# Kernel optimization log

Hardware: AMD Instinct MI355X
Metric: run time of the kernel (lower is better)

Reference implementation:

```python
import jax, jax.numpy as jnp
import numpy as np

TOP_K = 2  # moe_top_k


def setup_inputs() -> dict:
    key = jax.random.key(0)
    k0, k1, k2, k3 = jax.random.split(key, 4)
    SL, BS, H, F, E = 2048, 4, 1024, 1024, 8
    x = jax.random.normal(k0, (SL, BS, H), dtype=jnp.float32)
    w_router = jax.random.normal(k1, (H, E), dtype=jnp.float32) * 0.02
    w1 = jax.random.normal(k2, (E, H, F), dtype=jnp.float32) * 0.02  # per-expert map weights
    w2 = jax.random.normal(k3, (E, F, H), dtype=jnp.float32) * 0.02  # per-expert reduce weights
    return {"x": x, "w_router": w_router, "w1": w1, "w2": w2}


def reference(x, w_router, w1, w2):
    # dMoA forward: router -> dropless dispatch -> per-expert map GEMM ->
    # per-expert reduce GEMM -> expert-weighted combine. Dropless = no capacity
    # dropping, so a dense all-experts compute + per-token selection is exactly
    # equivalent in math to the sort/gather/grouped-GEMM/scatter pipeline.
    sl, bs, h = x.shape
    E = w1.shape[0]
    xt = x.reshape(-1, h)  # [T, H], T = sl*bs
    T = xt.shape[0]

    # LearnedRouter: softmax over expert logits, then top-k weights/indices
    scores = jax.nn.softmax(xt @ w_router, axis=-1)       # [T, E]
    expert_weights, top_experts = jax.lax.top_k(scores, TOP_K)  # [T, K]

    # load-balancing loss (router.loss): E * sum_e f_e * p_e
    onehot = jax.nn.one_hot(top_experts, E, dtype=xt.dtype)  # [T, K, E]
    tokens_frac = onehot.sum(axis=(0, 1)) / (T * TOP_K)      # f_e
    probs_mean = scores.mean(axis=0)                         # p_e
    loss = E * jnp.sum(tokens_frac * probs_mean)

    # map: per-expert linear H->F, select the top-k experts' outputs per token
    y_all = jnp.einsum('th,ehf->tef', xt, w1)                 # [T, E, F]
    h_tk = jnp.take_along_axis(y_all, top_experts[:, :, None], axis=1)  # [T, K, F]

    # reduce: weighted scatter-combine, then per-expert linear F->H
    hw = jnp.einsum('tke,tk,tkf->tef', onehot, expert_weights, h_tk)  # [T, E, F]
    out = jnp.einsum('tef,efh->th', hw, w2)                   # [T, H]
    return out.reshape(sl, bs, h), loss
```

## Files before the change

### kernel.cpp

```cpp
#include <hip/hip_runtime.h>
#include <hip/hip_bf16.h>
#include <stdint.h>


#define HD 1024
#define FD 1024
#define EN 8

typedef __attribute__((ext_vector_type(8))) short bf16x8;
typedef __attribute__((ext_vector_type(4))) float f32x4;

__device__ __forceinline__ void gload16(const void* g, void* l) {
    __builtin_amdgcn_global_load_lds(
        (const __attribute__((address_space(1))) unsigned int*)g,
        (__attribute__((address_space(3))) unsigned int*)l, 16, 0, 0);
}

__device__ __forceinline__ ushort f2bf(float v) {
    __hip_bfloat16 h = __float2bfloat16(v);
    return *(ushort*)&h;
}
__device__ __forceinline__ float bf2f(ushort u) {
    unsigned int w = ((unsigned int)u) << 16;
    float f; __builtin_memcpy(&f, &w, 4); return f;
}

__global__ __launch_bounds__(256) void router_kernel(
    const float* __restrict__ x, const float* __restrict__ wrt,
    ushort* __restrict__ xb,
    int* __restrict__ top_e, float* __restrict__ top_w,
    int* __restrict__ counts, float* __restrict__ probsum)
{
    __shared__ int   cnt_s[EN];
    __shared__ float ps_s[EN];
    int tid = threadIdx.x;
    if (tid < EN) { cnt_s[tid] = 0; ps_s[tid] = 0.f; }
    __syncthreads();

    int wid = tid >> 6, lane = tid & 63;
    int t = blockIdx.x * 4 + wid;
    const float4* xr4 = (const float4*)(x + (size_t)t * HD);
    ushort4* xbo = (ushort4*)(xb + (size_t)t * HD);
    float acc[EN];
#pragma unroll
    for (int e = 0; e < EN; e++) acc[e] = 0.f;
#pragma unroll
    for (int it = 0; it < 4; it++) {
        float4 xv = xr4[it * 64 + lane];
        ushort4 o; o.x = f2bf(xv.x); o.y = f2bf(xv.y); o.z = f2bf(xv.z); o.w = f2bf(xv.w);
        xbo[it * 64 + lane] = o;
        int h0 = it * 256 + lane * 4;
        float xs[4] = {xv.x, xv.y, xv.z, xv.w};
#pragma unroll
        for (int j = 0; j < 4; j++) {
            const float4* wp = (const float4*)(wrt + (size_t)(h0 + j) * EN);
            float4 wa = wp[0], wb = wp[1];
            acc[0] += xs[j] * wa.x; acc[1] += xs[j] * wa.y;
            acc[2] += xs[j] * wa.z; acc[3] += xs[j] * wa.w;
            acc[4] += xs[j] * wb.x; acc[5] += xs[j] * wb.y;
            acc[6] += xs[j] * wb.z; acc[7] += xs[j] * wb.w;
        }
    }
#pragma unroll
    for (int off = 32; off >= 1; off >>= 1) {
#pragma unroll
        for (int e = 0; e < EN; e++) acc[e] += __shfl_xor(acc[e], off, 64);
    }
    if (lane == 0) {
        float m = acc[0];
#pragma unroll
        for (int e = 1; e < EN; e++) m = fmaxf(m, acc[e]);
        float p[EN], s = 0.f;
#pragma unroll
        for (int e = 0; e < EN; e++) { p[e] = expf(acc[e] - m); s += p[e]; }
        float inv = 1.f / s;
#pragma unroll
        for (int e = 0; e < EN; e++) p[e] *= inv;
        int e0 = 0;
#pragma unroll
        for (int e = 1; e < EN; e++) if (p[e] > p[e0]) e0 = e;
        int e1 = (e0 == 0) ? 1 : 0;
#pragma unroll
        for (int e = 0; e < EN; e++) {
            if (e == e0) continue;
            if (p[e] > p[e1]) e1 = e;
        }
        top_e[t * 2] = e0;  top_e[t * 2 + 1] = e1;
        top_w[t * 2] = p[e0]; top_w[t * 2 + 1] = p[e1];
        atomicAdd(&cnt_s[e0], 1); atomicAdd(&cnt_s[e1], 1);
#pragma unroll
        for (int e = 0; e < EN; e++) atomicAdd(&ps_s[e], p[e]);
    }
    __syncthreads();
    if (tid < EN) {
        atomicAdd(&counts[tid], cnt_s[tid]);
        atomicAdd(&probsum[tid], ps_s[tid]);
    }
}

__global__ void prep_kernel(const int* __restrict__ counts,
                            const float* __restrict__ probsum,
                            int* __restrict__ offs, float* __restrict__ loss_out)
{
    int off = 0; float loss = 0.f;
    for (int e = 0; e < EN; e++) {
        offs[e] = off;
        off += counts[e];
        loss += ((float)counts[e] / 16384.f) * (probsum[e] / 8192.f);
    }
    offs[EN] = off;
    *loss_out = 8.f * loss;
}

__global__ __launch_bounds__(256) void dispatch_kernel(
    const int* __restrict__ top_e, const float* __restrict__ top_w,
    const int* __restrict__ offs, int* __restrict__ cursor,
    int* __restrict__ tok_list, float* __restrict__ w_list)
{
    int t = blockIdx.x * 256 + threadIdx.x;
    int lane = threadIdx.x & 63;
#pragma unroll
    for (int k = 0; k < 2; k++) {
        int e = top_e[t * 2 + k];
        int idx = 0;
#pragma unroll
        for (int ex = 0; ex < EN; ex++) {
            unsigned long long m = __ballot(e == ex);
            if (e == ex) {
                int cnt = __popcll(m);
                int leader = __ffsll(m) - 1;
                int pos = 0;
                if (lane == leader) pos = atomicAdd(&cursor[ex * 16], cnt);
                pos = __shfl(pos, leader, 64);
                int rank = __popcll(m & ((1ull << lane) - 1ull));
                idx = offs[ex] + pos + rank;
            }
        }
        tok_list[idx] = t * 2 + k;
        w_list[idx] = top_w[t * 2 + k];
    }
}

__global__ __launch_bounds__(256) void transpose_conv_kernel(
    const float* __restrict__ w1, const float* __restrict__ w2,
    ushort* __restrict__ w1b, ushort* __restrict__ w2b)
{
    __shared__ float tile[32][33];
    int bid = blockIdx.x;
    const float* in; ushort* outp;
    if (bid >= 8192) { in = w2; outp = w2b; bid -= 8192; }
    else             { in = w1; outp = w1b; }
    int e  = bid >> 10;
    int t2 = bid & 1023;
    int tb = t2 >> 5;
    int ta = t2 & 31;
    const float* pin = in + ((size_t)e << 20);
    ushort* pout = outp + ((size_t)e << 20);
    int tx = threadIdx.x & 31, ty = threadIdx.x >> 5;
#pragma unroll
    for (int j = 0; j < 4; j++)
        tile[ty + j * 8][tx] = pin[(size_t)(ta * 32 + ty + j * 8) * 1024 + tb * 32 + tx];
    __syncthreads();
#pragma unroll
    for (int j = 0; j < 4; j++)
        pout[(size_t)(tb * 32 + ty + j * 8) * 1024 + ta * 32 + tx] =
            f2bf(tile[tx][ty + j * 8]);
}


__global__ __launch_bounds__(512, 2) void map_gemm(
    const ushort* __restrict__ xb, const ushort* __restrict__ w1b,
    ushort* __restrict__ hbuf,
    const int* __restrict__ tok_list, const float* __restrict__ w_list,
    const int* __restrict__ offs)
{
    __shared__ __align__(16) short lA[2][256][64];
    __shared__ __align__(16) short lB[2][256][64];
    __shared__ int   tok_s[256];
    __shared__ float wt_s[256];

    int g = blockIdx.x;
    int e = g & 7, q = g >> 3, nb = q & 3, rb = q >> 2;
    int base = offs[e], cnt = offs[e + 1] - base;
    int row0 = rb << 8;
    if (row0 >= cnt) return;
    int rem = cnt - row0;
    int tid = threadIdx.x;
    if (tid < 256) {
        int r = row0 + tid; if (r > cnt - 1) r = cnt - 1;
        tok_s[tid] = tok_list[base + r];
        wt_s[tid]  = w_list[base + r];
    }
    __syncthreads();

    int lane = tid & 63, w = tid >> 6;
    int wm = w >> 2, wn = w & 3;
    int w32 = w * 32;
    int lr = lane >> 3;
    int kseg = ((lane & 7) ^ lr) << 3;

    const ushort* pA[4]; const ushort* pB[4];
    const ushort* wbase = w1b + ((size_t)e << 20);
#pragma unroll
    for (int i = 0; i < 4; i++) {
        int rowT = w32 + i * 8 + lr;
        pA[i] = xb + (size_t)(tok_s[rowT] >> 1) * HD + kseg;
        pB[i] = wbase + (size_t)(nb * 256 + rowT) * HD + kseg;
    }

    f32x4 acc[8][4];
#pragma unroll
    for (int m = 0; m < 8; m++)
#pragma unroll
        for (int n = 0; n < 4; n++) acc[m][n] = (f32x4){0.f, 0.f, 0.f, 0.f};

#pragma unroll
    for (int i = 0; i < 4; i++) {
        gload16(pA[i], &lA[0][w32 + i * 8][0]);
        gload16(pB[i], &lB[0][w32 + i * 8][0]);
        pA[i] += 64; pB[i] += 64;
    }
    __syncthreads();

    int lo = lane & 15, hi = lane >> 4, rx = lane & 7;
    for (int t = 0; t < 16; ++t) {
        int cur = t & 1;
        if (t < 15) {
            int nxt = cur ^ 1;
#pragma unroll
            for (int i = 0; i < 4; i++) {
                gload16(pA[i], &lA[nxt][w32 + i * 8][0]);
                gload16(pB[i], &lB[nxt][w32 + i * 8][0]);
                pA[i] += 64; pB[i] += 64;
            }
        }
#pragma unroll
        for (int ks = 0; ks < 2; ks++) {
            bf16x8 af[8], bg[4];
#pragma unroll
            for (int m = 0; m < 8; m++)
                af[m] = *(const bf16x8*)&lA[cur][wm * 128 + m * 16 + lo][((ks * 4 + hi) ^ rx) << 3];
#pragma unroll
            for (int n = 0; n < 4; n++)
                bg[n] = *(const bf16x8*)&lB[cur][wn * 64 + n * 16 + lo][((ks * 4 + hi) ^ rx) << 3];
#pragma unroll
            for (int m = 0; m < 8; m++)
#pragma unroll
                for (int n = 0; n < 4; n++)
                    acc[m][n] = __builtin_amdgcn_mfma_f32_16x16x32_bf16(af[m], bg[n], acc[m][n], 0, 0, 0);
        }
        __syncthreads();
    }

    short* ep = (w < 4 ? (short*)lA : (short*)lB) + (w & 3) * 8192;
#pragma unroll
    for (int m = 0; m < 8; m++)
#pragma unroll
        for (int r = 0; r < 4; r++) {
            int row_l = m * 16 + hi * 4 + r;
            int rswz = (row_l & 7) << 4;
            float wgt = wt_s[wm * 128 + row_l];
#pragma unroll
            for (int n = 0; n < 4; n++) {
                int colb = (n * 16 + lo) * 2;
                ep[(row_l * 128 + (colb ^ rswz)) >> 1] = f2bf(acc[m][n][r] * wgt);
            }
        }
    __syncthreads();
    size_t outbase = (size_t)(base + row0);
    int colg0 = (nb << 8) + wn * 64;
#pragma unroll
    for (int j = 0; j < 16; j++) {
        int row_l = j * 8 + (lane >> 3);
        int r_blk = wm * 128 + row_l;
        int sb = ((lane & 7) * 16) ^ ((row_l & 7) << 4);
        bf16x8 v = *(const bf16x8*)&ep[(row_l * 128 + sb) >> 1];
        if (r_blk < rem)
            *(bf16x8*)&hbuf[(outbase + r_blk) * FD + colg0 + (lane & 7) * 8] = v;
    }
}

__global__ __launch_bounds__(512, 2) void reduce_gemm(
    const ushort* __restrict__ hbuf, const ushort* __restrict__ w2b,
    ushort* __restrict__ obuf,
    const int* __restrict__ tok_list, const int* __restrict__ offs)
{
    __shared__ __align__(16) short lA[2][256][64];
    __shared__ __align__(16) short lB[2][256][64];
    __shared__ int tok_s[256];

    int g = blockIdx.x;
    int e = g & 7, q = g >> 3, nb = q & 3, rb = q >> 2;
    int base = offs[e], cnt = offs[e + 1] - base;
    int row0 = rb << 8;
    if (row0 >= cnt) return;
    int rem = cnt - row0;
    int tid = threadIdx.x;
    if (tid < 256) {
        int r = row0 + tid; if (r > cnt - 1) r = cnt - 1;
        tok_s[tid] = tok_list[base + r];
    }
    __syncthreads();

    int lane = tid & 63, w = tid >> 6;
    int wm = w >> 2, wn = w & 3;
    int w32 = w * 32;
    int lr = lane >> 3;
    int kseg = ((lane & 7) ^ lr) << 3;

    const ushort* pA[4]; const ushort* pB[4];
    const ushort* wbase = w2b + ((size_t)e << 20);
#pragma unroll
    for (int i = 0; i < 4; i++) {
        int rowT = w32 + i * 8 + lr;
        int ar = row0 + rowT; if (ar > cnt - 1) ar = cnt - 1;
        pA[i] = hbuf + (size_t)(base + ar) * FD + kseg;
        pB[i] = wbase + (size_t)(nb * 256 + rowT) * FD + kseg;
    }

    f32x4 acc[8][4];
#pragma unroll
    for (int m = 0; m < 8; m++)
#pragma unroll
        for (int n = 0; n < 4; n++) acc[m][n] = (f32x4){0.f, 0.f, 0.f, 0.f};

#pragma unroll
    for (int i = 0; i < 4; i++) {
        gload16(pA[i], &lA[0][w32 + i * 8][0]);
        gload16(pB[i], &lB[0][w32 + i * 8][0]);
        pA[i] += 64; pB[i] += 64;
    }
    __syncthreads();

    int lo = lane & 15, hi = lane >> 4, rx = lane & 7;
    for (int t = 0; t < 16; ++t) {
        int cur = t & 1;
        if (t < 15) {
            int nxt = cur ^ 1;
#pragma unroll
            for (int i = 0; i < 4; i++) {
                gload16(pA[i], &lA[nxt][w32 + i * 8][0]);
                gload16(pB[i], &lB[nxt][w32 + i * 8][0]);
                pA[i] += 64; pB[i] += 64;
            }
        }
#pragma unroll
        for (int ks = 0; ks < 2; ks++) {
            bf16x8 af[8], bg[4];
#pragma unroll
            for (int m = 0; m < 8; m++)
                af[m] = *(const bf16x8*)&lA[cur][wm * 128 + m * 16 + lo][((ks * 4 + hi) ^ rx) << 3];
#pragma unroll
            for (int n = 0; n < 4; n++)
                bg[n] = *(const bf16x8*)&lB[cur][wn * 64 + n * 16 + lo][((ks * 4 + hi) ^ rx) << 3];
#pragma unroll
            for (int m = 0; m < 8; m++)
#pragma unroll
                for (int n = 0; n < 4; n++)
                    acc[m][n] = __builtin_amdgcn_mfma_f32_16x16x32_bf16(af[m], bg[n], acc[m][n], 0, 0, 0);
        }
        __syncthreads();
    }

    short* ep = (w < 4 ? (short*)lA : (short*)lB) + (w & 3) * 8192;
#pragma unroll
    for (int m = 0; m < 8; m++)
#pragma unroll
        for (int r = 0; r < 4; r++) {
            int row_l = m * 16 + hi * 4 + r;
            int rswz = (row_l & 7) << 4;
#pragma unroll
            for (int n = 0; n < 4; n++) {
                int colb = (n * 16 + lo) * 2;
                ep[(row_l * 128 + (colb ^ rswz)) >> 1] = f2bf(acc[m][n][r]);
            }
        }
    __syncthreads();
    int colg0 = (nb << 8) + wn * 64;
#pragma unroll
    for (int j = 0; j < 16; j++) {
        int row_l = j * 8 + (lane >> 3);
        int r_blk = wm * 128 + row_l;
        int sb = ((lane & 7) * 16) ^ ((row_l & 7) << 4);
        bf16x8 v = *(const bf16x8*)&ep[(row_l * 128 + sb) >> 1];
        if (r_blk < rem)
            *(bf16x8*)&obuf[(size_t)tok_s[r_blk] * HD + colg0 + (lane & 7) * 8] = v;
    }
}

__global__ __launch_bounds__(256) void combine_kernel(
    const ushort* __restrict__ obuf, float* __restrict__ out)
{
    int g = blockIdx.x * 256 + threadIdx.x;
    int t = g >> 7, c8 = (g & 127) << 3;
    const ushort* p = obuf + (size_t)t * 2048 + c8;
    bf16x8 a = *(const bf16x8*)p;
    bf16x8 b = *(const bf16x8*)(p + 1024);
    float o[8];
#pragma unroll
    for (int i = 0; i < 8; i++)
        o[i] = bf2f((ushort)a[i]) + bf2f((ushort)b[i]);
    float* q = out + (size_t)t * HD + c8;
    *(float4*)q       = (float4){o[0], o[1], o[2], o[3]};
    *(float4*)(q + 4) = (float4){o[4], o[5], o[6], o[7]};
}

extern "C" void kernel_launch(void* const* d_in, const int* in_sizes, int n_in,
                              void* d_out, int out_size, void* d_ws, size_t ws_size,
                              hipStream_t stream)
{
    const float* x   = (const float*)d_in[0];
    const float* wrt = (const float*)d_in[1];
    const float* w1  = (const float*)d_in[2];
    const float* w2  = (const float*)d_in[3];
    float* out = (float*)d_out;

    uint8_t* ws = (uint8_t*)d_ws;
    ushort* xb   = (ushort*)(ws);
    ushort* w1b  = (ushort*)(ws + (16u << 20));
    ushort* obuf = (ushort*)(ws);
    ushort* w2b  = (ushort*)(ws + (32u << 20));
    ushort* hbuf = (ushort*)(ws + (48u << 20));
    uint8_t* p80 = ws + (80u << 20);
    int*   tok_list = (int*)(p80);
    float* w_list   = (float*)(p80 + (64u << 10));
    int*   top_e    = (int*)(p80 + (128u << 10));
    float* top_w    = (float*)(p80 + (192u << 10));
    uint8_t* ctr    = p80 + (256u << 10);
    int*   counts   = (int*)(ctr);
    float* probsum  = (float*)(ctr + 64);
    int*   offs     = (int*)(ctr + 128);
    int*   cursor   = (int*)(ctr + 256);
    float* loss_out = out + 8388608;

    hipMemsetAsync(ctr, 0, 1024, stream);

    router_kernel<<<2048, 256, 0, stream>>>(x, wrt, xb, top_e, top_w, counts, probsum);
    prep_kernel<<<1, 1, 0, stream>>>(counts, probsum, offs, loss_out);
    dispatch_kernel<<<32, 256, 0, stream>>>(top_e, top_w, offs, cursor, tok_list, w_list);
    transpose_conv_kernel<<<16384, 256, 0, stream>>>(w1, w2, w1b, w2b);
    map_gemm<<<1024, 512, 0, stream>>>(xb, w1b, hbuf, tok_list, w_list, offs);
    reduce_gemm<<<1024, 512, 0, stream>>>(hbuf, w2b, obuf, tok_list, offs);
    combine_kernel<<<4096, 256, 0, stream>>>(obuf, out);
}
```

Measured before the change: 225.4 us.

## Deepen GEMM pipeline to 4-stage K=32 ring with explicit waitcnt scheduling

Both the map and reduce grouped GEMMs change from a 2-stage double buffer with K=64 tiles to a 4-deep ring of K=32 stages. Three stages are kept in flight and each step waits on vmcnt with an explicit barrier. The inner step uses inline ds_read_b128, sched_barriers, and s_setprio around the MFMA bursts so that LDS reads interleave with matrix work and global loads stay hidden. A new XOR swizzle matches the 32-element row layout. The hand scheduling removes compiler freedom and depends on the vmcnt counts being exact.

```diff
diff --git a/kernel.cpp b/kernel.cpp
--- a/kernel.cpp
+++ b/kernel.cpp
@@ -14,6 +14,14 @@
     __builtin_amdgcn_global_load_lds(
         (const __attribute__((address_space(1))) unsigned int*)g,
         (__attribute__((address_space(3))) unsigned int*)l, 16, 0, 0);
+}
+
+__device__ __forceinline__ bf16x8 ds_read128(const short* p) {
+    bf16x8 r;
+    asm volatile("ds_read_b128 %0, %1"
+                 : "=v"(r)
+                 : "v"((const __attribute__((address_space(3))) short*)p));
+    return r;
 }
 
 __device__ __forceinline__ ushort f2bf(float v) {
@@ -168,14 +176,51 @@
 }
 
 
+#define RDA_(r_, m_) ds_read128((const short*)&L[r_][0][wm * 128 + (m_) * 16 + lo][pslot])
+#define RDB_(r_, n_) ds_read128((const short*)&L[r_][1][wn * 64  + (n_) * 16 + lo][pslot])
+
+#define STAGE(h_) do {                                                        \
+    int r_ = (h_) & 3; int ko_ = (h_) << 5;                                   \
+    gload16(pA0 + ko_, &L[r_][0][w16][0]);                                    \
+    gload16(pA1 + ko_, &L[r_][0][128 + w16][0]);                              \
+    gload16(pB0 + ko_, &L[r_][1][w16][0]);                                    \
+    gload16(pB1 + ko_, &L[r_][1][128 + w16][0]);                              \
+} while (0)
+
+#define KHALF(r_, VMSTR) do {                                                 \
+    asm volatile("s_waitcnt vmcnt(" VMSTR ")" ::: "memory");                  \
+    __builtin_amdgcn_s_barrier();                                             \
+    __builtin_amdgcn_sched_barrier(0);                                        \
+    _Pragma("unroll") for (int m = 0; m < 4; m++) a[m] = RDA_(r_, m);         \
+    _Pragma("unroll") for (int n = 0; n < 4; n++) b[n] = RDB_(r_, n);         \
+    asm volatile("s_waitcnt lgkmcnt(0)");                                     \
+    __builtin_amdgcn_sched_barrier(0);                                        \
+    __builtin_amdgcn_s_setprio(1);                                            \
+    _Pragma("unroll") for (int m = 0; m < 4; m++)                             \
+    _Pragma("unroll") for (int n = 0; n < 4; n++)                             \
+        acc[m][n] = __builtin_amdgcn_mfma_f32_16x16x32_bf16(a[m], b[n], acc[m][n], 0, 0, 0); \
+    __builtin_amdgcn_s_setprio(0);                                            \
+    __builtin_amdgcn_sched_barrier(0);                                        \
+    _Pragma("unroll") for (int m = 0; m < 4; m++) a[m] = RDA_(r_, m + 4);     \
+    asm volatile("s_waitcnt lgkmcnt(0)");                                     \
+    __builtin_amdgcn_sched_barrier(0);                                        \
+    __builtin_amdgcn_s_setprio(1);                                            \
+    _Pragma("unroll") for (int m = 0; m < 4; m++)                             \
+    _Pragma("unroll") for (int n = 0; n < 4; n++)                             \
+        acc[m + 4][n] = __builtin_amdgcn_mfma_f32_16x16x32_bf16(a[m], b[n], acc[m + 4][n], 0, 0, 0); \
+    __builtin_amdgcn_s_setprio(0);                                            \
+    __builtin_amdgcn_sched_barrier(0);                                        \
+    __builtin_amdgcn_s_barrier();                        \
+    __builtin_amdgcn_sched_barrier(0);                                        \
+} while (0)
+
 __global__ __launch_bounds__(512, 2) void map_gemm(
     const ushort* __restrict__ xb, const ushort* __restrict__ w1b,
     ushort* __restrict__ hbuf,
     const int* __restrict__ tok_list, const float* __restrict__ w_list,
     const int* __restrict__ offs)
 {
-    __shared__ __align__(16) short lA[2][256][64];
-    __shared__ __align__(16) short lB[2][256][64];
+    __shared__ __align__(16) short L[4][2][256][32];
     __shared__ int   tok_s[256];
     __shared__ float wt_s[256];
 
@@ -195,18 +240,17 @@
 
     int lane = tid & 63, w = tid >> 6;
     int wm = w >> 2, wn = w & 3;
-    int w32 = w * 32;
-    int lr = lane >> 3;
-    int kseg = ((lane & 7) ^ lr) << 3;
-
-    const ushort* pA[4]; const ushort* pB[4];
+    int w16 = w * 16;
+    int lo = lane & 15, hi = lane >> 4;
+    int pslot = (hi ^ ((lo >> 1) & 3)) << 3;
+
+    int rowA = tid >> 2;
+    int ksw  = ((tid & 3) ^ ((tid >> 3) & 3)) << 3;
     const ushort* wbase = w1b + ((size_t)e << 20);
-#pragma unroll
-    for (int i = 0; i < 4; i++) {
-        int rowT = w32 + i * 8 + lr;
-        pA[i] = xb + (size_t)(tok_s[rowT] >> 1) * HD + kseg;
-        pB[i] = wbase + (size_t)(nb * 256 + rowT) * HD + kseg;
-    }
+    const ushort* pA0 = xb + (size_t)(tok_s[rowA] >> 1) * HD + ksw;
+    const ushort* pA1 = xb + (size_t)(tok_s[rowA + 128] >> 1) * HD + ksw;
+    const ushort* pB0 = wbase + (size_t)(nb * 256 + rowA) * HD + ksw;
+    const ushort* pB1 = wbase + (size_t)(nb * 256 + rowA + 128) * HD + ksw;
 
     f32x4 acc[8][4];
 #pragma unroll
@@ -214,45 +258,19 @@
 #pragma unroll
         for (int n = 0; n < 4; n++) acc[m][n] = (f32x4){0.f, 0.f, 0.f, 0.f};
 
-#pragma unroll
-    for (int i = 0; i < 4; i++) {
-        gload16(pA[i], &lA[0][w32 + i * 8][0]);
-        gload16(pB[i], &lB[0][w32 + i * 8][0]);
-        pA[i] += 64; pB[i] += 64;
-    }
-    __syncthreads();
-
-    int lo = lane & 15, hi = lane >> 4, rx = lane & 7;
-    for (int t = 0; t < 16; ++t) {
-        int cur = t & 1;
-        if (t < 15) {
-            int nxt = cur ^ 1;
-#pragma unroll
-            for (int i = 0; i < 4; i++) {
-                gload16(pA[i], &lA[nxt][w32 + i * 8][0]);
-                gload16(pB[i], &lB[nxt][w32 + i * 8][0]);
-                pA[i] += 64; pB[i] += 64;
-            }
-        }
-#pragma unroll
-        for (int ks = 0; ks < 2; ks++) {
-            bf16x8 af[8], bg[4];
-#pragma unroll
-            for (int m = 0; m < 8; m++)
-                af[m] = *(const bf16x8*)&lA[cur][wm * 128 + m * 16 + lo][((ks * 4 + hi) ^ rx) << 3];
-#pragma unroll
-            for (int n = 0; n < 4; n++)
-                bg[n] = *(const bf16x8*)&lB[cur][wn * 64 + n * 16 + lo][((ks * 4 + hi) ^ rx) << 3];
-#pragma unroll
-            for (int m = 0; m < 8; m++)
-#pragma unroll
-                for (int n = 0; n < 4; n++)
-                    acc[m][n] = __builtin_amdgcn_mfma_f32_16x16x32_bf16(af[m], bg[n], acc[m][n], 0, 0, 0);
-        }
-        __syncthreads();
-    }
-
-    short* ep = (w < 4 ? (short*)lA : (short*)lB) + (w & 3) * 8192;
+    bf16x8 a[4], b[4];
+
+    STAGE(0); STAGE(1); STAGE(2);
+    for (int h = 0; h < 29; h++) {
+        STAGE(h + 3);
+        int r = h & 3;
+        KHALF(r, "12");
+    }
+    KHALF(1, "8");
+    KHALF(2, "4");
+    KHALF(3, "0");
+
+    short* ep = (short*)L + w * 8192;
 #pragma unroll
     for (int m = 0; m < 8; m++)
 #pragma unroll
@@ -285,8 +303,7 @@
     ushort* __restrict__ obuf,
     const int* __restrict__ tok_list, const int* __restrict__ offs)
 {
-    __shared__ __align__(16) short lA[2][256][64];
-    __shared__ __align__(16) short lB[2][256][64];
+    __shared__ __align__(16) short L[4][2][256][32];
     __shared__ int tok_s[256];
 
     int g = blockIdx.x;
@@ -304,19 +321,19 @@
 
     int lane = tid & 63, w = tid >> 6;
     int wm = w >> 2, wn = w & 3;
-    int w32 = w * 32;
-    int lr = lane >> 3;
-    int kseg = ((lane & 7) ^ lr) << 3;
-
-    const ushort* pA[4]; const ushort* pB[4];
+    int w16 = w * 16;
+    int lo = lane & 15, hi = lane >> 4;
+    int pslot = (hi ^ ((lo >> 1) & 3)) << 3;
+
+    int rowA = tid >> 2;
+    int ksw  = ((tid & 3) ^ ((tid >> 3) & 3)) << 3;
+    int ar0 = row0 + rowA;        if (ar0 > cnt - 1) ar0 = cnt - 1;
+    int ar1 = row0 + rowA + 128;  if (ar1 > cnt - 1) ar1 = cnt - 1;
     const ushort* wbase = w2b + ((size_t)e << 20);
-#pragma unroll
-    for (int i = 0; i < 4; i++) {
-        int rowT = w32 + i * 8 + lr;
-        int ar = row0 + rowT; if (ar > cnt - 1) ar = cnt - 1;
-        pA[i] = hbuf + (size_t)(base + ar) * FD + kseg;
-        pB[i] = wbase + (size_t)(nb * 256 + rowT) * FD + kseg;
-    }
+    const ushort* pA0 = hbuf + (size_t)(base + ar0) * FD + ksw;
+    const ushort* pA1 = hbuf + (size_t)(base + ar1) * FD + ksw;
+    const ushort* pB0 = wbase + (size_t)(nb * 256 + rowA) * FD + ksw;
+    const ushort* pB1 = wbase + (size_t)(nb * 256 + rowA + 128) * FD + ksw;
 
     f32x4 acc[8][4];
 #pragma unroll
@@ -324,45 +341,19 @@
 #pragma unroll
         for (int n = 0; n < 4; n++) acc[m][n] = (f32x4){0.f, 0.f, 0.f, 0.f};
 
-#pragma unroll
-    for (int i = 0; i < 4; i++) {
-        gload16(pA[i], &lA[0][w32 + i * 8][0]);
-        gload16(pB[i], &lB[0][w32 + i * 8][0]);
-        pA[i] += 64; pB[i] += 64;
-    }
-    __syncthreads();
-
-    int lo = lane & 15, hi = lane >> 4, rx = lane & 7;
-    for (int t = 0; t < 16; ++t) {
-        int cur = t & 1;
-        if (t < 15) {
-            int nxt = cur ^ 1;
-#pragma unroll
-            for (int i = 0; i < 4; i++) {
-                gload16(pA[i], &lA[nxt][w32 + i * 8][0]);
-                gload16(pB[i], &lB[nxt][w32 + i * 8][0]);
-                pA[i] += 64; pB[i] += 64;
-            }
-        }
-#pragma unroll
-        for (int ks = 0; ks < 2; ks++) {
-            bf16x8 af[8], bg[4];
-#pragma unroll
-            for (int m = 0; m < 8; m++)
-                af[m] = *(const bf16x8*)&lA[cur][wm * 128 + m * 16 + lo][((ks * 4 + hi) ^ rx) << 3];
-#pragma unroll
-            for (int n = 0; n < 4; n++)
-                bg[n] = *(const bf16x8*)&lB[cur][wn * 64 + n * 16 + lo][((ks * 4 + hi) ^ rx) << 3];
-#pragma unroll
-            for (int m = 0; m < 8; m++)
-#pragma unroll
-                for (int n = 0; n < 4; n++)
-                    acc[m][n] = __builtin_amdgcn_mfma_f32_16x16x32_bf16(af[m], bg[n], acc[m][n], 0, 0, 0);
-        }
-        __syncthreads();
-    }
-
-    short* ep = (w < 4 ? (short*)lA : (short*)lB) + (w & 3) * 8192;
+    bf16x8 a[4], b[4];
+
+    STAGE(0); STAGE(1); STAGE(2);
+    for (int h = 0; h < 29; h++) {
+        STAGE(h + 3);
+        int r = h & 3;
+        KHALF(r, "12");
+    }
+    KHALF(1, "8");
+    KHALF(2, "4");
+    KHALF(3, "0");
+
+    short* ep = (short*)L + w * 8192;
 #pragma unroll
     for (int m = 0; m < 8; m++)
 #pragma unroll
```

New measurement: 223.6 us. About the same (-0.8%).
